# Performance work log

Measured on AMD Instinct MI355X. Metric: run time of the kernel, lower is better.

Reference implementation:

```python
import jax, jax.numpy as jnp
import numpy as np

B, T, H, HW = 16, 32, 512, 32  # batch, timesteps, hidden channels, spatial size


def setup_inputs() -> dict:
    key = jax.random.key(0)
    k1, k2, k3, k4, k5 = jax.random.split(key, 5)
    x = jax.random.normal(k1, (B, T, HW, HW), dtype=jnp.float32)
    # cell conv: 1x1, (1 + H) -> 4H, with bias (k=1 default, padding 'same')
    W_conv = jax.random.normal(k2, (4 * H, 1 + H, 1, 1), dtype=jnp.float32) * 0.02
    b_conv = jax.random.normal(k3, (4 * H,), dtype=jnp.float32) * 0.02
    # post conv: 3x3, H -> 1, padding 'same'
    W_post = jax.random.normal(k4, (1, H, 3, 3), dtype=jnp.float32) * 0.02
    b_post = jax.random.normal(k5, (1,), dtype=jnp.float32) * 0.02
    return {"x": x, "W_conv": W_conv, "b_conv": b_conv, "W_post": W_post, "b_post": b_post}


def _post_conv(h, W_post, b_post):
    # NCHW 3x3 'same' conv
    y = jax.lax.conv_general_dilated(
        h, W_post, window_strides=(1, 1), padding="SAME",
        dimension_numbers=("NCHW", "OIHW", "NCHW"))
    return y + b_post[None, :, None, None]


def reference(x, W_conv, b_conv, W_post, b_post):
    Wc = W_conv[:, :, 0, 0]  # [4H, 1+H] -- 1x1 conv is a channel GEMM

    def step(carry, xt):
        h, c = carry  # [B,H,32,32] each; xt [B,1,32,32]
        z = jnp.concatenate([xt, h], axis=1)  # [B,1+H,32,32]
        gates = jnp.einsum("bchw,oc->bohw", z, Wc) + b_conv[None, :, None, None]
        i, f, o, g = jnp.split(gates, 4, axis=1)
        # Faithful to source (non-standard gating):
        c = jax.nn.sigmoid(f) * c + jax.nn.sigmoid(i) + jnp.tanh(g)
        h = jax.nn.sigmoid(o) + jnp.tanh(c)
        y = _post_conv(h, W_post, b_post)  # [B,1,32,32]
        return (h, c), y

    h0 = jnp.zeros((x.shape[0], H, HW, HW), dtype=x.dtype)
    c0 = jnp.zeros_like(h0)
    xs = x[:, :, None, :, :].transpose(1, 0, 2, 3, 4)  # [T,B,1,32,32]
    _, ys = jax.lax.scan(step, (h0, c0), xs)  # ys [T,B,1,32,32]
    out = ys[:, :, 0].transpose(1, 0, 2, 3)  # [B,T,32,32] == cat along dim=1
    return out
```

## Files before the change

kernel.cpp:

```cpp
#include <hip/hip_runtime.h>
#include <cstdint>
#include <cstddef>

#define B_    16
#define T_    32
#define H_    512
#define P_    1024
#define NPOS  16384
#define NG    2048

typedef __attribute__((ext_vector_type(8))) short short8;
typedef __attribute__((ext_vector_type(4))) float f32x4;

__device__ __forceinline__ unsigned short f2bf(float f) {
  uint32_t u = __float_as_uint(f);
  u += 0x7fffu + ((u >> 16) & 1u);
  return (unsigned short)(u >> 16);
}
__device__ __forceinline__ float bflo(uint32_t u) { return __uint_as_float(u << 16); }
__device__ __forceinline__ float bfhi(uint32_t u) { return __uint_as_float(u & 0xffff0000u); }

__device__ __forceinline__ float sigf(float x) {
  return __builtin_amdgcn_rcpf(1.0f + __expf(-x));
}
__device__ __forceinline__ float tanhf_(float x) {
  return 1.0f - 2.0f * __builtin_amdgcn_rcpf(__expf(2.0f * x) + 1.0f);
}

__device__ __forceinline__ void gload_lds16(const void* g, void* l) {
  __builtin_amdgcn_global_load_lds(
      (const __attribute__((address_space(1))) void*)g,
      (__attribute__((address_space(3))) void*)l, 16, 0, 0);
}

__global__ void repack_w(const float* __restrict__ Wc, const float* __restrict__ bconv,
                         unsigned short* __restrict__ Wp, float* __restrict__ w0x,
                         float* __restrict__ bx) {
  int idx = blockIdx.x * 256 + threadIdx.x;
  int r = idx >> 9, k = idx & 511;
  int ch = r >> 2, g = r & 3;
  int o = g * 512 + ch;
  Wp[idx] = f2bf(Wc[o * 513 + 1 + k]);
  if (k == 0) { w0x[r] = Wc[o * 513]; bx[r] = bconv[o]; }
}

__global__ void repack_wpost(const float* __restrict__ Wpost, float* __restrict__ wpp) {
  int idx = blockIdx.x * 256 + threadIdx.x;
  if (idx >= 9 * 512) return;
  int j = idx >> 9, c = idx & 511;
  wpp[idx] = Wpost[c * 9 + j];
}

__global__ __launch_bounds__(512, 2)
void lstm_step(const unsigned short* __restrict__ Wp,
               const unsigned short* __restrict__ hprev,
               unsigned short* __restrict__ hnext,
               _Float16* __restrict__ Cst,
               const float* __restrict__ w0x, const float* __restrict__ bxv,
               const float* __restrict__ xin, int t) {
  __shared__ unsigned short As[2][256 * 64];
  __shared__ unsigned short Bs[2][256 * 64];

  const int tid = threadIdx.x;
  const int lane = tid & 63;
  const int wv = tid >> 6;
  const int wm = wv >> 2, wn = wv & 3;
  const int q = lane >> 4, l = lane & 15;

  const int bid = blockIdx.x;
  const int xcd = bid & 7;
  const int slot = bid >> 3;
  const int ny = xcd * 8 + (slot & 7);
  const int rx = slot >> 3;
  const int r0 = rx * 256;
  const int n0 = ny * 256;

  const int srow = tid >> 3;
  const int lchunk = (tid & 7) ^ (srow & 7);
  const unsigned short* gA = Wp    + (size_t)(r0 + srow) * 512 + lchunk * 8;
  const unsigned short* gB = hprev + (size_t)(n0 + srow) * 512 + lchunk * 8;

  f32x4 acc[8][4] = {};

  auto stage = [&](int bb, int kc) {
    char* lA = (char*)As[bb] + wv * 1024;
    char* lB = (char*)Bs[bb] + wv * 1024;
#pragma unroll
    for (int j = 0; j < 4; ++j) {
      gload_lds16(gA + (size_t)j * (64 * 512) + kc, lA + j * 8192);
      gload_lds16(gB + (size_t)j * (64 * 512) + kc, lB + j * 8192);
    }
  };

  stage(0, 0);

#pragma unroll
  for (int kt = 0; kt < 8; ++kt) {
    const int cur = kt & 1;
    if (kt < 7) {
      stage(cur ^ 1, (kt + 1) * 64);
      asm volatile("s_waitcnt vmcnt(8)" ::: "memory");
    } else {
      asm volatile("s_waitcnt vmcnt(0)" ::: "memory");
    }
    __builtin_amdgcn_s_barrier();

#pragma unroll
    for (int kk = 0; kk < 2; ++kk) {
      short8 af[8], bf_[4];
#pragma unroll
      for (int mi = 0; mi < 8; ++mi) {
        int row = wm * 128 + mi * 16 + l;
        int sidx = row * 64 + (((kk * 4 + q) ^ (row & 7)) * 8);
        af[mi] = *(const short8*)(As[cur] + sidx);
      }
#pragma unroll
      for (int ni = 0; ni < 4; ++ni) {
        int row = wn * 64 + ni * 16 + l;
        int sidx = row * 64 + (((kk * 4 + q) ^ (row & 7)) * 8);
        bf_[ni] = *(const short8*)(Bs[cur] + sidx);
      }
      __builtin_amdgcn_s_setprio(1);
#pragma unroll
      for (int mi = 0; mi < 8; ++mi)
#pragma unroll
        for (int ni = 0; ni < 4; ++ni)
          acc[mi][ni] = __builtin_amdgcn_mfma_f32_16x16x32_bf16(af[mi], bf_[ni], acc[mi][ni], 0, 0, 0);
      __builtin_amdgcn_s_setprio(0);
      __builtin_amdgcn_s_barrier();
    }
  }

  float xv[4]; int posL[4]; size_t cbase[4];
#pragma unroll
  for (int ni = 0; ni < 4; ++ni) {
    posL[ni] = wn * 64 + ni * 16 + l;
    int pos = n0 + posL[ni];
    int b = pos >> 10, p = pos & 1023;
    xv[ni] = xin[((b * T_ + t) << 10) + p];
    cbase[ni] = ((size_t)b << 19) + p;
  }
  const int ch0 = rx * 64;
#pragma unroll
  for (int mi = 0; mi < 8; ++mi) {
    int chl = wm * 32 + mi * 4 + q;
    int rg = r0 + wm * 128 + mi * 16 + q * 4;
    float4 w0 = *(const float4*)(w0x + rg);
    float4 bb = *(const float4*)(bxv + rg);
    int ch = ch0 + chl;
#pragma unroll
    for (int ni = 0; ni < 4; ++ni) {
      f32x4 g = acc[mi][ni];
      float gi = g[0] + w0.x * xv[ni] + bb.x;
      float gf = g[1] + w0.y * xv[ni] + bb.y;
      float go = g[2] + w0.z * xv[ni] + bb.z;
      float gg = g[3] + w0.w * xv[ni] + bb.w;
      size_t cidx = cbase[ni] + ((size_t)ch << 10);
      float cold = (float)Cst[cidx];
      float cn = sigf(gf) * cold + sigf(gi) + tanhf_(gg);
      float hn = sigf(go) + tanhf_(cn);
      Cst[cidx] = (_Float16)cn;
      As[0][posL[ni] * 64 + (chl ^ ((posL[ni] & 7) << 3))] = f2bf(hn);
    }
  }
  __syncthreads();
  {
    int pl = tid >> 1;
    int cb = (tid & 1) << 2;
    const unsigned short* srcrow = As[0] + pl * 64;
    unsigned short* dst = hnext + (size_t)(n0 + pl) * 512 + ch0 + (cb << 3);
#pragma unroll
    for (int i = 0; i < 4; ++i)
      ((uint4*)dst)[i] = *(const uint4*)(srcrow + (((cb + i) ^ (pl & 7)) << 3));
  }
}

__global__ __launch_bounds__(256)
void post_conv(const unsigned short* __restrict__ h, const float* __restrict__ wpp,
               const float* __restrict__ bpost, float* __restrict__ out, int t) {
  int wid = blockIdx.x * 4 + (threadIdx.x >> 6);
  int lane = threadIdx.x & 63;
  int b = wid >> 10, p = wid & 1023;
  int py = p >> 5, px = p & 31;
  int c0 = lane << 3;
  float acc = 0.f;
#pragma unroll
  for (int dy = -1; dy <= 1; ++dy) {
    int ny = py + dy;
    if ((unsigned)ny > 31u) continue;
#pragma unroll
    for (int dx = -1; dx <= 1; ++dx) {
      int nx = px + dx;
      if ((unsigned)nx > 31u) continue;
      int j = (dy + 1) * 3 + (dx + 1);
      const uint4 hv = *(const uint4*)(h + ((size_t)((b << 10) + (ny << 5) + nx) << 9) + c0);
      const float4 wa = *(const float4*)(wpp + (j << 9) + c0);
      const float4 wb = *(const float4*)(wpp + (j << 9) + c0 + 4);
      acc += bflo(hv.x) * wa.x + bfhi(hv.x) * wa.y
           + bflo(hv.y) * wa.z + bfhi(hv.y) * wa.w
           + bflo(hv.z) * wb.x + bfhi(hv.z) * wb.y
           + bflo(hv.w) * wb.z + bfhi(hv.w) * wb.w;
    }
  }
#pragma unroll
  for (int off = 1; off < 64; off <<= 1)
    acc += __shfl_xor(acc, off, 64);
  if (lane == 0)
    out[((b * T_ + t) << 10) + p] = acc + bpost[0];
}

extern "C" void kernel_launch(void* const* d_in, const int* in_sizes, int n_in,
                              void* d_out, int out_size, void* d_ws, size_t ws_size,
                              hipStream_t stream) {
  const float* x     = (const float*)d_in[0];
  const float* Wconv = (const float*)d_in[1];
  const float* bconv = (const float*)d_in[2];
  const float* Wpost = (const float*)d_in[3];
  const float* bpost = (const float*)d_in[4];
  float* out = (float*)d_out;
  char* ws = (char*)d_ws;

  unsigned short* h0  = (unsigned short*)(ws);
  unsigned short* h1  = (unsigned short*)(ws + 16777216);
  _Float16*       Cst = (_Float16*)(ws + 33554432);
  unsigned short* Wp  = (unsigned short*)(ws + 50331648);
  float*          w0x = (float*)(ws + 52428800);
  float*          bx  = (float*)(ws + 52436992);
  float*          wpp = (float*)(ws + 52445184);

  hipMemsetAsync(h0, 0, 16777216, stream);
  hipMemsetAsync(Cst, 0, 16777216, stream);
  repack_w<<<4096, 256, 0, stream>>>(Wconv, bconv, Wp, w0x, bx);
  repack_wpost<<<18, 256, 0, stream>>>(Wpost, wpp);

  unsigned short* hp = h0;
  unsigned short* hn = h1;
  for (int t = 0; t < T_; ++t) {
    lstm_step<<<512, 512, 0, stream>>>(Wp, hp, hn, Cst, w0x, bx, x, t);
    post_conv<<<4096, 256, 0, stream>>>(hn, wpp, bpost, out, t);
    unsigned short* tmp = hp; hp = hn; hn = tmp;
  }
}
```

Before: 2.122 ms.

## Restructure GEMM mainloop into 4-stage K=32 pipeline with split A/B staging

Replaces the double-buffered K=64 tile loop in the LSTM gate GEMM with a four-deep ring of K=32 slices, prefetching three slices ahead. Loads of A and B are interleaved between two half-MFMA phases, with finer vmcnt waits and extra barriers. The aim is to hide global-to-LDS latency and spread LDS reads across MFMA work. The cost is twice as many barriers per K, plus a new swizzle layout that has to stay conflict-free.

```diff
diff --git a/kernel.cpp b/kernel.cpp
--- a/kernel.cpp
+++ b/kernel.cpp
@@ -58,8 +58,8 @@
                _Float16* __restrict__ Cst,
                const float* __restrict__ w0x, const float* __restrict__ bxv,
                const float* __restrict__ xin, int t) {
-  __shared__ unsigned short As[2][256 * 64];
-  __shared__ unsigned short Bs[2][256 * 64];
+  __shared__ unsigned short As[4 * 256 * 32];
+  __shared__ unsigned short Bs[4 * 256 * 32];
 
   const int tid = threadIdx.x;
   const int lane = tid & 63;
@@ -69,66 +69,84 @@
 
   const int bid = blockIdx.x;
   const int xcd = bid & 7;
-  const int slot = bid >> 3;
-  const int ny = xcd * 8 + (slot & 7);
-  const int rx = slot >> 3;
-  const int r0 = rx * 256;
-  const int n0 = ny * 256;
-
-  const int srow = tid >> 3;
-  const int lchunk = (tid & 7) ^ (srow & 7);
-  const unsigned short* gA = Wp    + (size_t)(r0 + srow) * 512 + lchunk * 8;
-  const unsigned short* gB = hprev + (size_t)(n0 + srow) * 512 + lchunk * 8;
+  const int sl  = bid >> 3;
+  const int ny  = xcd * 8 + (sl & 7);
+  const int rx  = sl >> 3;
+  const int r0  = rx * 256;
+  const int n0  = ny * 256;
+
+  const int rr = wv * 16 + (lane >> 2);
+  const int gchunk = (lane & 3) ^ (rr & 3);
+  const unsigned short* gAsrc = Wp    + (size_t)(r0 + rr) * 512 + gchunk * 8;
+  const unsigned short* gBsrc = hprev + (size_t)(n0 + rr) * 512 + gchunk * 8;
+  char* ldA = (char*)As + wv * 1024;
+  char* ldB = (char*)Bs + wv * 1024;
+
+  auto stageA = [&](int hf) {
+    char* d = ldA + (hf & 3) * 16384;
+    gload_lds16(gAsrc + hf * 32, d);
+    gload_lds16(gAsrc + 128 * 512 + hf * 32, d + 8192);
+  };
+  auto stageB = [&](int hf) {
+    char* d = ldB + (hf & 3) * 16384;
+    gload_lds16(gBsrc + hf * 32, d);
+    gload_lds16(gBsrc + 128 * 512 + hf * 32, d + 8192);
+  };
 
   f32x4 acc[8][4] = {};
 
-  auto stage = [&](int bb, int kc) {
-    char* lA = (char*)As[bb] + wv * 1024;
-    char* lB = (char*)Bs[bb] + wv * 1024;
-#pragma unroll
-    for (int j = 0; j < 4; ++j) {
-      gload_lds16(gA + (size_t)j * (64 * 512) + kc, lA + j * 8192);
-      gload_lds16(gB + (size_t)j * (64 * 512) + kc, lB + j * 8192);
-    }
-  };
-
-  stage(0, 0);
-
-#pragma unroll
-  for (int kt = 0; kt < 8; ++kt) {
-    const int cur = kt & 1;
-    if (kt < 7) {
-      stage(cur ^ 1, (kt + 1) * 64);
-      asm volatile("s_waitcnt vmcnt(8)" ::: "memory");
-    } else {
-      asm volatile("s_waitcnt vmcnt(0)" ::: "memory");
-    }
-    __builtin_amdgcn_s_barrier();
-
-#pragma unroll
-    for (int kk = 0; kk < 2; ++kk) {
-      short8 af[8], bf_[4];
-#pragma unroll
-      for (int mi = 0; mi < 8; ++mi) {
-        int row = wm * 128 + mi * 16 + l;
-        int sidx = row * 64 + (((kk * 4 + q) ^ (row & 7)) * 8);
-        af[mi] = *(const short8*)(As[cur] + sidx);
-      }
-#pragma unroll
-      for (int ni = 0; ni < 4; ++ni) {
-        int row = wn * 64 + ni * 16 + l;
-        int sidx = row * 64 + (((kk * 4 + q) ^ (row & 7)) * 8);
-        bf_[ni] = *(const short8*)(Bs[cur] + sidx);
-      }
-      __builtin_amdgcn_s_setprio(1);
-#pragma unroll
-      for (int mi = 0; mi < 8; ++mi)
-#pragma unroll
-        for (int ni = 0; ni < 4; ++ni)
-          acc[mi][ni] = __builtin_amdgcn_mfma_f32_16x16x32_bf16(af[mi], bf_[ni], acc[mi][ni], 0, 0, 0);
-      __builtin_amdgcn_s_setprio(0);
-      __builtin_amdgcn_s_barrier();
-    }
+  const int cxb = (q ^ (l & 3)) << 4;
+
+  stageA(0); stageB(0); stageA(1); stageB(1); stageA(2); stageB(2);
+  asm volatile("s_waitcnt vmcnt(8)" ::: "memory");
+  __builtin_amdgcn_s_barrier();
+
+#pragma unroll
+  for (int h = 0; h < 16; ++h) {
+    const char* Ah = (const char*)As + (h & 3) * 16384;
+    const char* Bh = (const char*)Bs + (h & 3) * 16384;
+
+    short8 a0[4], b_[4];
+#pragma unroll
+    for (int mi = 0; mi < 4; ++mi) {
+      int row = wm * 128 + mi * 16 + l;
+      a0[mi] = *(const short8*)(Ah + row * 64 + cxb);
+    }
+#pragma unroll
+    for (int ni = 0; ni < 4; ++ni) {
+      int row = wn * 64 + ni * 16 + l;
+      b_[ni] = *(const short8*)(Bh + row * 64 + cxb);
+    }
+    if (h + 3 < 16) stageA(h + 3);
+    __builtin_amdgcn_s_barrier();
+    __builtin_amdgcn_s_setprio(1);
+#pragma unroll
+    for (int mi = 0; mi < 4; ++mi)
+#pragma unroll
+      for (int ni = 0; ni < 4; ++ni)
+        acc[mi][ni] = __builtin_amdgcn_mfma_f32_16x16x32_bf16(a0[mi], b_[ni], acc[mi][ni], 0, 0, 0);
+    __builtin_amdgcn_s_setprio(0);
+    __builtin_amdgcn_s_barrier();
+
+    short8 a1[4];
+#pragma unroll
+    for (int mi = 0; mi < 4; ++mi) {
+      int row = wm * 128 + (mi + 4) * 16 + l;
+      a1[mi] = *(const short8*)(Ah + row * 64 + cxb);
+    }
+    if (h + 3 < 16) stageB(h + 3);
+    if (h <= 12)      asm volatile("s_waitcnt vmcnt(8)" ::: "memory");
+    else if (h == 13) asm volatile("s_waitcnt vmcnt(4)" ::: "memory");
+    else if (h == 14) asm volatile("s_waitcnt vmcnt(0)" ::: "memory");
+    __builtin_amdgcn_s_barrier();
+    __builtin_amdgcn_s_setprio(1);
+#pragma unroll
+    for (int mi = 0; mi < 4; ++mi)
+#pragma unroll
+      for (int ni = 0; ni < 4; ++ni)
+        acc[mi + 4][ni] = __builtin_amdgcn_mfma_f32_16x16x32_bf16(a1[mi], b_[ni], acc[mi + 4][ni], 0, 0, 0);
+    __builtin_amdgcn_s_setprio(0);
+    __builtin_amdgcn_s_barrier();
   }
 
   float xv[4]; int posL[4]; size_t cbase[4];
@@ -160,14 +178,14 @@
       float cn = sigf(gf) * cold + sigf(gi) + tanhf_(gg);
       float hn = sigf(go) + tanhf_(cn);
       Cst[cidx] = (_Float16)cn;
-      As[0][posL[ni] * 64 + (chl ^ ((posL[ni] & 7) << 3))] = f2bf(hn);
+      As[posL[ni] * 64 + (chl ^ ((posL[ni] & 7) << 3))] = f2bf(hn);
     }
   }
   __syncthreads();
   {
     int pl = tid >> 1;
     int cb = (tid & 1) << 2;
-    const unsigned short* srcrow = As[0] + pl * 64;
+    const unsigned short* srcrow = As + pl * 64;
     unsigned short* dst = hnext + (size_t)(n0 + pl) * 512 + ch0 + (cb << 3);
 #pragma unroll
     for (int i = 0; i < 4; ++i)
```

New measurement: 2.269 ms. 1.07x slower.
